# Performance work log

Hardware: AMD Instinct MI355X
Metric: run time of the kernel (lower is better)

Reference implementation:

```python
import jax, jax.numpy as jnp
import numpy as np

B = 32          # decode batch (one new token each)
KV = 4096       # kv-cache length per sequence
H = 4096        # hidden_size
NH = 32         # num query heads
NKV = 8         # num kv heads
D = 128         # head_dim
G = NH // NKV   # GQA group size
EPS = 1e-6
THETA = 1000000.0
SCALE = D ** -0.5


def _rmsnorm(x, w):
    var = jnp.mean(x * x, axis=-1, keepdims=True)
    return x * jax.lax.rsqrt(var + EPS) * w


def setup_inputs() -> dict:
    key = jax.random.key(0)
    ks = jax.random.split(key, 6)
    hidden_states = jax.random.normal(ks[0], (B, H), jnp.float32)
    k_buffer = jax.random.normal(ks[1], (B, KV, NKV, D), jnp.float32)
    v_buffer = jax.random.normal(ks[2], (B, KV, NKV, D), jnp.float32)
    wqkv = jax.random.normal(ks[3], ((NH + 2 * NKV) * D, H), jnp.float32) * 0.02
    wo = jax.random.normal(ks[4], (H, NH * D), jnp.float32) * 0.02
    q_norm_w = jnp.ones((D,), jnp.float32)
    k_norm_w = jnp.ones((D,), jnp.float32)
    # new token sits at the last cache slot; positions = kv_len-1
    position_ids = jnp.full((B,), KV - 1, jnp.int32)
    out_cache_loc = jnp.full((B,), KV - 1, jnp.int32)
    return {
        "position_ids": position_ids,
        "hidden_states": hidden_states,
        "k_buffer": k_buffer,
        "v_buffer": v_buffer,
        "out_cache_loc": out_cache_loc,
        "wqkv": wqkv,
        "wo": wo,
        "q_norm_w": q_norm_w,
        "k_norm_w": k_norm_w,
    }


def reference(position_ids, hidden_states, k_buffer, v_buffer, out_cache_loc,
              wqkv, wo, q_norm_w, k_norm_w):
    # fused QKV projection (no bias)
    qkv = hidden_states @ wqkv.T                               # [B, (NH+2NKV)*D]
    q = qkv[:, : NH * D].reshape(B, NH, D)
    k = qkv[:, NH * D : (NH + NKV) * D].reshape(B, NKV, D)
    v = qkv[:, (NH + NKV) * D :].reshape(B, NKV, D)

    # per-head RMSNorm on q and k
    q = _rmsnorm(q, q_norm_w)
    k = _rmsnorm(k, k_norm_w)

    # NeoX-style rotary embedding
    inv_freq = 1.0 / (THETA ** (jnp.arange(0, D, 2, dtype=jnp.float32) / D))
    freqs = position_ids.astype(jnp.float32)[:, None] * inv_freq  # [B, D/2]
    cos = jnp.cos(freqs)[:, None, :]
    sin = jnp.sin(freqs)[:, None, :]

    def rot(x):
        x1, x2 = jnp.split(x, 2, axis=-1)
        return jnp.concatenate([x1 * cos - x2 * sin, x2 * cos + x1 * sin], -1)

    q = rot(q)
    k = rot(k)

    # fused_set_kv_buffer: scatter roped k and pre-rope v into the cache
    b = jnp.arange(B)
    k_buffer = k_buffer.at[b, out_cache_loc].set(k)            # [B, KV, NKV, D]
    v_buffer = v_buffer.at[b, out_cache_loc].set(v)

    # GQA attention over the full cache (decode: all slots valid)
    qg = q.reshape(B, NKV, G, D)
    scores = jnp.einsum('bkgd,bskd->bkgs', qg, k_buffer) * SCALE  # [B,NKV,G,KV]
    p = jax.nn.softmax(scores, axis=-1)
    o = jnp.einsum('bkgs,bskd->bkgd', p, v_buffer).reshape(B, NH * D)

    return o @ wo.T                                            # [B, H]
```

## Files before the change

kernel.cpp:

```cpp
#include <hip/hip_runtime.h>
#include <math.h>
#include <stdint.h>

#define B_ 32
#define KV_LEN 4096
#define HID 4096
#define NH 32
#define NKV 8
#define HD 128
#define GQ 4
#define EPS 1e-6f
#define THETA 1000000.0f
#define SCALE 0.08838834764831845f
#define QKV_ROWS ((NH + 2 * NKV) * HD)
#define SPLITS 8
#define SCHUNK (KV_LEN / SPLITS)

__global__ __launch_bounds__(256, 2)
void gemm_bt(const float* __restrict__ A, const float* __restrict__ Wt,
             float* __restrict__ out, int K, int ld_out) {
    __shared__ float sh[32][256];
    const int tid  = threadIdx.x;
    const int wave = tid >> 6;
    const int lane = tid & 63;
    const int jg   = (wave & 1) * 4;
    const int bg   = (wave >> 1) * 16;
    const int j0   = blockIdx.x * 8;

    float acc[4][16];
#pragma unroll
    for (int j = 0; j < 4; ++j)
#pragma unroll
        for (int b = 0; b < 16; ++b) acc[j][b] = 0.0f;

    for (int kc = 0; kc < K; kc += 256) {
#pragma unroll
        for (int i = 0; i < 8; ++i) {
            int f   = tid + i * 256;
            int row = f >> 6;
            int c4  = f & 63;
            *reinterpret_cast<float4*>(&sh[row][c4 * 4]) =
                *reinterpret_cast<const float4*>(&A[(size_t)row * K + kc + c4 * 4]);
        }
        __syncthreads();

        float4 w4[4];
#pragma unroll
        for (int j = 0; j < 4; ++j)
            w4[j] = *reinterpret_cast<const float4*>(
                &Wt[(size_t)(j0 + jg + j) * K + kc + lane * 4]);

#pragma unroll
        for (int b = 0; b < 16; ++b) {
            float4 h4 = *reinterpret_cast<const float4*>(&sh[bg + b][lane * 4]);
#pragma unroll
            for (int j = 0; j < 4; ++j)
                acc[j][b] += w4[j].x * h4.x + w4[j].y * h4.y +
                             w4[j].z * h4.z + w4[j].w * h4.w;
        }
        __syncthreads();
    }

#pragma unroll
    for (int j = 0; j < 4; ++j) {
#pragma unroll
        for (int b = 0; b < 16; ++b) {
            float v = acc[j][b];
#pragma unroll
            for (int m = 1; m < 64; m <<= 1) v += __shfl_xor(v, m);
            if (lane == j * 16 + b)
                out[(size_t)(bg + b) * ld_out + j0 + jg + j] = v;
        }
    }
}

__global__ __launch_bounds__(64)
void qkv_post(const float* __restrict__ qkv, const int* __restrict__ pos_ids,
              const int* __restrict__ out_loc, const float* __restrict__ qw,
              const float* __restrict__ kw, float* __restrict__ qbuf,
              float* __restrict__ kbuf, float* __restrict__ vbuf) {
    const int head = blockIdx.x;
    const int b    = blockIdx.y;
    const int i    = threadIdx.x;
    const float* row = qkv + (size_t)b * QKV_ROWS + head * HD;
    float x1 = row[i], x2 = row[i + 64];

    if (head >= NH + NKV) {
        int kh  = head - NH - NKV;
        int loc = out_loc[b];
        float* dst = vbuf + (((size_t)b * KV_LEN + loc) * NKV + kh) * HD;
        dst[i] = x1;
        dst[i + 64] = x2;
        return;
    }

    float ss = x1 * x1 + x2 * x2;
#pragma unroll
    for (int m = 1; m < 64; m <<= 1) ss += __shfl_xor(ss, m);
    float r = rsqrtf(ss * (1.0f / 128.0f) + EPS);
    const float* w = (head < NH) ? qw : kw;
    float y1 = x1 * r * w[i];
    float y2 = x2 * r * w[i + 64];

    float pos = (float)pos_ids[b];
    float inv_freq = expf(-(logf(THETA) / 64.0f) * (float)i);
    float ang = pos * inv_freq;
    float c = cosf(ang), s = sinf(ang);
    float o1 = y1 * c - y2 * s;
    float o2 = y2 * c + y1 * s;

    if (head < NH) {
        float* dst = qbuf + ((size_t)b * NH + head) * HD;
        dst[i] = o1;
        dst[i + 64] = o2;
    } else {
        int kh  = head - NH;
        int loc = out_loc[b];
        float* dst = kbuf + (((size_t)b * KV_LEN + loc) * NKV + kh) * HD;
        dst[i] = o1;
        dst[i + 64] = o2;
    }
}

__global__ __launch_bounds__(256, 4)
void attn_decode(const float* __restrict__ qbuf, const float* __restrict__ kbuf,
                 const float* __restrict__ vbuf, float* __restrict__ part_o,
                 float* __restrict__ part_m, float* __restrict__ part_l) {
    const int split = blockIdx.x, h = blockIdx.y, b = blockIdx.z;
    const int tid = threadIdx.x;
    const int grp = tid >> 4;
    const int i   = tid & 15;

    float4 qa[GQ], qb[GQ];
#pragma unroll
    for (int g = 0; g < GQ; ++g) {
        const float* qp = qbuf + ((size_t)b * NH + h * GQ + g) * HD;
        qa[g] = *reinterpret_cast<const float4*>(qp + 4 * i);
        qb[g] = *reinterpret_cast<const float4*>(qp + 64 + 4 * i);
    }

    float m[GQ], l[GQ];
    float4 oa[GQ], ob[GQ];
#pragma unroll
    for (int g = 0; g < GQ; ++g) {
        m[g] = -1e30f;
        l[g] = 0.0f;
        oa[g] = make_float4(0.f, 0.f, 0.f, 0.f);
        ob[g] = make_float4(0.f, 0.f, 0.f, 0.f);
    }

    const int s0 = split * SCHUNK;
    for (int t = 0; t < SCHUNK / 16; ++t) {
        const int s = s0 + t * 16 + grp;
        const float* krow = kbuf + (((size_t)b * KV_LEN + s) * NKV + h) * HD;
        const float* vrow = vbuf + (((size_t)b * KV_LEN + s) * NKV + h) * HD;
        float4 ka = *reinterpret_cast<const float4*>(krow + 4 * i);
        float4 kb = *reinterpret_cast<const float4*>(krow + 64 + 4 * i);
        float4 va = *reinterpret_cast<const float4*>(vrow + 4 * i);
        float4 vb = *reinterpret_cast<const float4*>(vrow + 64 + 4 * i);

#pragma unroll
        for (int g = 0; g < GQ; ++g) {
            float d = ka.x * qa[g].x + ka.y * qa[g].y + ka.z * qa[g].z + ka.w * qa[g].w +
                      kb.x * qb[g].x + kb.y * qb[g].y + kb.z * qb[g].z + kb.w * qb[g].w;
            d += __shfl_xor(d, 1);
            d += __shfl_xor(d, 2);
            d += __shfl_xor(d, 4);
            d += __shfl_xor(d, 8);
            float sc = d * SCALE;
            float mn = fmaxf(m[g], sc);
            float p    = __expf(sc - mn);
            float corr = __expf(m[g] - mn);
            l[g] = l[g] * corr + p;
            oa[g].x = oa[g].x * corr + p * va.x;
            oa[g].y = oa[g].y * corr + p * va.y;
            oa[g].z = oa[g].z * corr + p * va.z;
            oa[g].w = oa[g].w * corr + p * va.w;
            ob[g].x = ob[g].x * corr + p * vb.x;
            ob[g].y = ob[g].y * corr + p * vb.y;
            ob[g].z = ob[g].z * corr + p * vb.z;
            ob[g].w = ob[g].w * corr + p * vb.w;
            m[g] = mn;
        }
    }

    __shared__ float smo[16][GQ][HD];
    __shared__ float smm[16][GQ];
    __shared__ float sml[16][GQ];
#pragma unroll
    for (int g = 0; g < GQ; ++g) {
        if (i == 0) { smm[grp][g] = m[g]; sml[grp][g] = l[g]; }
        smo[grp][g][4 * i + 0] = oa[g].x;
        smo[grp][g][4 * i + 1] = oa[g].y;
        smo[grp][g][4 * i + 2] = oa[g].z;
        smo[grp][g][4 * i + 3] = oa[g].w;
        smo[grp][g][64 + 4 * i + 0] = ob[g].x;
        smo[grp][g][64 + 4 * i + 1] = ob[g].y;
        smo[grp][g][64 + 4 * i + 2] = ob[g].z;
        smo[grp][g][64 + 4 * i + 3] = ob[g].w;
    }
    __syncthreads();

    for (int idx = tid; idx < GQ * HD; idx += 256) {
        int g = idx >> 7, d = idx & 127;
        float mstar = -1e30f;
#pragma unroll
        for (int r = 0; r < 16; ++r) mstar = fmaxf(mstar, smm[r][g]);
        float L = 0.0f, o = 0.0f;
#pragma unroll
        for (int r = 0; r < 16; ++r) {
            float w = __expf(smm[r][g] - mstar);
            L += w * sml[r][g];
            o += w * smo[r][g][d];
        }
        size_t pbase = (((size_t)b * NKV + h) * SPLITS + split) * GQ + g;
        part_o[pbase * HD + d] = o;
        if (d == 0) { part_m[pbase] = mstar; part_l[pbase] = L; }
    }
}

__global__ __launch_bounds__(128)
void attn_combine(const float* __restrict__ part_o, const float* __restrict__ part_m,
                  const float* __restrict__ part_l, float* __restrict__ attn_out) {
    const int h = blockIdx.x, b = blockIdx.y;
    const int d = threadIdx.x;
#pragma unroll
    for (int g = 0; g < GQ; ++g) {
        float mstar = -1e30f;
#pragma unroll
        for (int s = 0; s < SPLITS; ++s) {
            size_t p = (((size_t)b * NKV + h) * SPLITS + s) * GQ + g;
            mstar = fmaxf(mstar, part_m[p]);
        }
        float L = 0.0f, o = 0.0f;
#pragma unroll
        for (int s = 0; s < SPLITS; ++s) {
            size_t p = (((size_t)b * NKV + h) * SPLITS + s) * GQ + g;
            float w = __expf(part_m[p] - mstar);
            L += w * part_l[p];
            o += w * part_o[p * HD + d];
        }
        attn_out[(size_t)b * (NH * HD) + (h * GQ + g) * HD + d] = o / L;
    }
}

extern "C" void kernel_launch(void* const* d_in, const int* in_sizes, int n_in,
                              void* d_out, int out_size, void* d_ws, size_t ws_size,
                              hipStream_t stream) {
    const int*   pos    = (const int*)d_in[0];
    const float* hidden = (const float*)d_in[1];
    float*       kbuf   = (float*)d_in[2];
    float*       vbuf   = (float*)d_in[3];
    const int*   loc    = (const int*)d_in[4];
    const float* wqkv   = (const float*)d_in[5];
    const float* wo     = (const float*)d_in[6];
    const float* qnw    = (const float*)d_in[7];
    const float* knw    = (const float*)d_in[8];
    float*       out    = (float*)d_out;

    float* ws     = (float*)d_ws;
    float* qkv    = ws;
    float* qbuf   = qkv + (size_t)B_ * QKV_ROWS;
    float* part_o = qbuf + (size_t)B_ * NH * HD;
    float* part_m = part_o + (size_t)B_ * NKV * SPLITS * GQ * HD;
    float* part_l = part_m + (size_t)B_ * NKV * SPLITS * GQ;
    float* attn   = part_l + (size_t)B_ * NKV * SPLITS * GQ;

    gemm_bt<<<QKV_ROWS / 8, 256, 0, stream>>>(hidden, wqkv, qkv, HID, QKV_ROWS);
    qkv_post<<<dim3(NH + 2 * NKV, B_), 64, 0, stream>>>(qkv, pos, loc, qnw, knw,
                                                        qbuf, kbuf, vbuf);
    attn_decode<<<dim3(SPLITS, NKV, B_), 256, 0, stream>>>(qbuf, kbuf, vbuf,
                                                           part_o, part_m, part_l);
    attn_combine<<<dim3(NKV, B_), 128, 0, stream>>>(part_o, part_m, part_l, attn);
    gemm_bt<<<HID / 8, 256, 0, stream>>>(attn, wo, out, HID, HID);
}
```

Baseline: 1.166 ms.

## Double-buffer GEMM activations, prefetch KV rows, avoid cache writes, shuffle-reduce attention

The GEMM now stages activation tiles through a double-buffered LDS using global_load_lds and writes its output with one coalesced store per lane. Attention no longer scatters the new k/v into the input cache. It reads them from small side buffers when the slot matches out_cache_loc, prefetches the next K/V rows in registers, and folds SCALE into q. The per-block softmax merge uses wave shuffles before a smaller shared-memory merge. Occupancy is lowered to 3 blocks to make room for the extra prefetch registers. The cost is more register pressure, and the caller's KV cache buffers are no longer updated.

```diff
diff --git a/kernel.cpp b/kernel.cpp
--- a/kernel.cpp
+++ b/kernel.cpp
@@ -15,11 +15,12 @@
 #define QKV_ROWS ((NH + 2 * NKV) * HD)
 #define SPLITS 8
 #define SCHUNK (KV_LEN / SPLITS)
+#define NT (SCHUNK / 16)
 
 __global__ __launch_bounds__(256, 2)
 void gemm_bt(const float* __restrict__ A, const float* __restrict__ Wt,
              float* __restrict__ out, int K, int ld_out) {
-    __shared__ float sh[32][256];
+    __shared__ __align__(16) float sh[2][32][256];
     const int tid  = threadIdx.x;
     const int wave = tid >> 6;
     const int lane = tid & 63;
@@ -33,17 +34,30 @@
 #pragma unroll
         for (int b = 0; b < 16; ++b) acc[j][b] = 0.0f;
 
-    for (int kc = 0; kc < K; kc += 256) {
-#pragma unroll
-        for (int i = 0; i < 8; ++i) {
-            int f   = tid + i * 256;
-            int row = f >> 6;
-            int c4  = f & 63;
-            *reinterpret_cast<float4*>(&sh[row][c4 * 4]) =
-                *reinterpret_cast<const float4*>(&A[(size_t)row * K + kc + c4 * 4]);
-        }
-        __syncthreads();
-
+    const int nk = K >> 8;
+
+#pragma unroll
+    for (int i = 0; i < 8; ++i) {
+        const int row = 4 * i + wave;
+        __builtin_amdgcn_global_load_lds(
+            (const __attribute__((address_space(1))) void*)(A + (size_t)row * K + lane * 4),
+            (__attribute__((address_space(3))) void*)&sh[0][row][0], 16, 0, 0);
+    }
+    __syncthreads();
+
+    for (int c = 0; c < nk; ++c) {
+        const int cur = c & 1;
+        if (c + 1 < nk) {
+            const int kcn = (c + 1) << 8;
+#pragma unroll
+            for (int i = 0; i < 8; ++i) {
+                const int row = 4 * i + wave;
+                __builtin_amdgcn_global_load_lds(
+                    (const __attribute__((address_space(1))) void*)(A + (size_t)row * K + kcn + lane * 4),
+                    (__attribute__((address_space(3))) void*)&sh[cur ^ 1][row][0], 16, 0, 0);
+            }
+        }
+        const int kc = c << 8;
         float4 w4[4];
 #pragma unroll
         for (int j = 0; j < 4; ++j)
@@ -52,7 +66,7 @@
 
 #pragma unroll
         for (int b = 0; b < 16; ++b) {
-            float4 h4 = *reinterpret_cast<const float4*>(&sh[bg + b][lane * 4]);
+            float4 h4 = *reinterpret_cast<const float4*>(&sh[cur][bg + b][lane * 4]);
 #pragma unroll
             for (int j = 0; j < 4; ++j)
                 acc[j][b] += w4[j].x * h4.x + w4[j].y * h4.y +
@@ -61,6 +75,7 @@
         __syncthreads();
     }
 
+    float myv = 0.0f;
 #pragma unroll
     for (int j = 0; j < 4; ++j) {
 #pragma unroll
@@ -68,17 +83,17 @@
             float v = acc[j][b];
 #pragma unroll
             for (int m = 1; m < 64; m <<= 1) v += __shfl_xor(v, m);
-            if (lane == j * 16 + b)
-                out[(size_t)(bg + b) * ld_out + j0 + jg + j] = v;
-        }
-    }
+            if (lane == j * 16 + b) myv = v;
+        }
+    }
+    out[(size_t)(bg + (lane & 15)) * ld_out + j0 + jg + (lane >> 4)] = myv;
 }
 
 __global__ __launch_bounds__(64)
 void qkv_post(const float* __restrict__ qkv, const int* __restrict__ pos_ids,
-              const int* __restrict__ out_loc, const float* __restrict__ qw,
-              const float* __restrict__ kw, float* __restrict__ qbuf,
-              float* __restrict__ kbuf, float* __restrict__ vbuf) {
+              const float* __restrict__ qw, const float* __restrict__ kw,
+              float* __restrict__ qbuf, float* __restrict__ knew,
+              float* __restrict__ vnew) {
     const int head = blockIdx.x;
     const int b    = blockIdx.y;
     const int i    = threadIdx.x;
@@ -86,9 +101,7 @@
     float x1 = row[i], x2 = row[i + 64];
 
     if (head >= NH + NKV) {
-        int kh  = head - NH - NKV;
-        int loc = out_loc[b];
-        float* dst = vbuf + (((size_t)b * KV_LEN + loc) * NKV + kh) * HD;
+        float* dst = vnew + ((size_t)b * NKV + (head - NH - NKV)) * HD;
         dst[i] = x1;
         dst[i + 64] = x2;
         return;
@@ -111,25 +124,27 @@
 
     if (head < NH) {
         float* dst = qbuf + ((size_t)b * NH + head) * HD;
+        dst[i] = o1 * SCALE;
+        dst[i + 64] = o2 * SCALE;
+    } else {
+        float* dst = knew + ((size_t)b * NKV + (head - NH)) * HD;
         dst[i] = o1;
         dst[i + 64] = o2;
-    } else {
-        int kh  = head - NH;
-        int loc = out_loc[b];
-        float* dst = kbuf + (((size_t)b * KV_LEN + loc) * NKV + kh) * HD;
-        dst[i] = o1;
-        dst[i + 64] = o2;
-    }
-}
-
-__global__ __launch_bounds__(256, 4)
+    }
+}
+
+__global__ __launch_bounds__(256, 3)
 void attn_decode(const float* __restrict__ qbuf, const float* __restrict__ kbuf,
-                 const float* __restrict__ vbuf, float* __restrict__ part_o,
-                 float* __restrict__ part_m, float* __restrict__ part_l) {
+                 const float* __restrict__ vbuf, const float* __restrict__ knew,
+                 const float* __restrict__ vnew, const int* __restrict__ out_loc,
+                 float* __restrict__ part_o, float* __restrict__ part_m,
+                 float* __restrict__ part_l) {
     const int split = blockIdx.x, h = blockIdx.y, b = blockIdx.z;
-    const int tid = threadIdx.x;
-    const int grp = tid >> 4;
-    const int i   = tid & 15;
+    const int tid  = threadIdx.x;
+    const int wave = tid >> 6;
+    const int grp  = tid >> 4;
+    const int i    = tid & 15;
+    const int loc  = out_loc[b];
 
     float4 qa[GQ], qb[GQ];
 #pragma unroll
@@ -143,21 +158,32 @@
     float4 oa[GQ], ob[GQ];
 #pragma unroll
     for (int g = 0; g < GQ; ++g) {
-        m[g] = -1e30f;
-        l[g] = 0.0f;
+        m[g] = -1e30f; l[g] = 0.0f;
         oa[g] = make_float4(0.f, 0.f, 0.f, 0.f);
         ob[g] = make_float4(0.f, 0.f, 0.f, 0.f);
     }
 
+    const float* kn = knew + ((size_t)b * NKV + h) * HD;
+    const float* vn = vnew + ((size_t)b * NKV + h) * HD;
     const int s0 = split * SCHUNK;
-    for (int t = 0; t < SCHUNK / 16; ++t) {
-        const int s = s0 + t * 16 + grp;
-        const float* krow = kbuf + (((size_t)b * KV_LEN + s) * NKV + h) * HD;
-        const float* vrow = vbuf + (((size_t)b * KV_LEN + s) * NKV + h) * HD;
-        float4 ka = *reinterpret_cast<const float4*>(krow + 4 * i);
-        float4 kb = *reinterpret_cast<const float4*>(krow + 64 + 4 * i);
-        float4 va = *reinterpret_cast<const float4*>(vrow + 4 * i);
-        float4 vb = *reinterpret_cast<const float4*>(vrow + 64 + 4 * i);
+
+    int s = s0 + grp;
+    const float* kr = (s == loc) ? kn : kbuf + (((size_t)b * KV_LEN + s) * NKV + h) * HD;
+    const float* vr = (s == loc) ? vn : vbuf + (((size_t)b * KV_LEN + s) * NKV + h) * HD;
+    float4 ka = *reinterpret_cast<const float4*>(kr + 4 * i);
+    float4 kb = *reinterpret_cast<const float4*>(kr + 64 + 4 * i);
+    float4 va = *reinterpret_cast<const float4*>(vr + 4 * i);
+    float4 vb = *reinterpret_cast<const float4*>(vr + 64 + 4 * i);
+
+    for (int t = 0; t < NT; ++t) {
+        const int tn = (t + 1 < NT) ? t + 1 : t;
+        const int sn = s0 + tn * 16 + grp;
+        const float* krn = (sn == loc) ? kn : kbuf + (((size_t)b * KV_LEN + sn) * NKV + h) * HD;
+        const float* vrn = (sn == loc) ? vn : vbuf + (((size_t)b * KV_LEN + sn) * NKV + h) * HD;
+        float4 ka_n = *reinterpret_cast<const float4*>(krn + 4 * i);
+        float4 kb_n = *reinterpret_cast<const float4*>(krn + 64 + 4 * i);
+        float4 va_n = *reinterpret_cast<const float4*>(vrn + 4 * i);
+        float4 vb_n = *reinterpret_cast<const float4*>(vrn + 64 + 4 * i);
 
 #pragma unroll
         for (int g = 0; g < GQ; ++g) {
@@ -167,55 +193,78 @@
             d += __shfl_xor(d, 2);
             d += __shfl_xor(d, 4);
             d += __shfl_xor(d, 8);
-            float sc = d * SCALE;
-            float mn = fmaxf(m[g], sc);
-            float p    = __expf(sc - mn);
+            float mn   = fmaxf(m[g], d);
+            float p    = __expf(d - mn);
             float corr = __expf(m[g] - mn);
             l[g] = l[g] * corr + p;
-            oa[g].x = oa[g].x * corr + p * va.x;
-            oa[g].y = oa[g].y * corr + p * va.y;
-            oa[g].z = oa[g].z * corr + p * va.z;
-            oa[g].w = oa[g].w * corr + p * va.w;
-            ob[g].x = ob[g].x * corr + p * vb.x;
-            ob[g].y = ob[g].y * corr + p * vb.y;
-            ob[g].z = ob[g].z * corr + p * vb.z;
-            ob[g].w = ob[g].w * corr + p * vb.w;
+            oa[g].x = fmaf(oa[g].x, corr, p * va.x);
+            oa[g].y = fmaf(oa[g].y, corr, p * va.y);
+            oa[g].z = fmaf(oa[g].z, corr, p * va.z);
+            oa[g].w = fmaf(oa[g].w, corr, p * va.w);
+            ob[g].x = fmaf(ob[g].x, corr, p * vb.x);
+            ob[g].y = fmaf(ob[g].y, corr, p * vb.y);
+            ob[g].z = fmaf(ob[g].z, corr, p * vb.z);
+            ob[g].w = fmaf(ob[g].w, corr, p * vb.w);
             m[g] = mn;
         }
-    }
-
-    __shared__ float smo[16][GQ][HD];
-    __shared__ float smm[16][GQ];
-    __shared__ float sml[16][GQ];
-#pragma unroll
-    for (int g = 0; g < GQ; ++g) {
-        if (i == 0) { smm[grp][g] = m[g]; sml[grp][g] = l[g]; }
-        smo[grp][g][4 * i + 0] = oa[g].x;
-        smo[grp][g][4 * i + 1] = oa[g].y;
-        smo[grp][g][4 * i + 2] = oa[g].z;
-        smo[grp][g][4 * i + 3] = oa[g].w;
-        smo[grp][g][64 + 4 * i + 0] = ob[g].x;
-        smo[grp][g][64 + 4 * i + 1] = ob[g].y;
-        smo[grp][g][64 + 4 * i + 2] = ob[g].z;
-        smo[grp][g][64 + 4 * i + 3] = ob[g].w;
+        ka = ka_n; kb = kb_n; va = va_n; vb = vb_n;
+    }
+
+#pragma unroll
+    for (int off = 16; off <= 32; off <<= 1) {
+#pragma unroll
+        for (int g = 0; g < GQ; ++g) {
+            float mo = __shfl_xor(m[g], off);
+            float lo = __shfl_xor(l[g], off);
+            float M  = fmaxf(m[g], mo);
+            float cs = __expf(m[g] - M);
+            float co = __expf(mo - M);
+            l[g] = l[g] * cs + lo * co;
+            float4 t;
+            t.x = __shfl_xor(oa[g].x, off); t.y = __shfl_xor(oa[g].y, off);
+            t.z = __shfl_xor(oa[g].z, off); t.w = __shfl_xor(oa[g].w, off);
+            oa[g].x = oa[g].x * cs + t.x * co; oa[g].y = oa[g].y * cs + t.y * co;
+            oa[g].z = oa[g].z * cs + t.z * co; oa[g].w = oa[g].w * cs + t.w * co;
+            t.x = __shfl_xor(ob[g].x, off); t.y = __shfl_xor(ob[g].y, off);
+            t.z = __shfl_xor(ob[g].z, off); t.w = __shfl_xor(ob[g].w, off);
+            ob[g].x = ob[g].x * cs + t.x * co; ob[g].y = ob[g].y * cs + t.y * co;
+            ob[g].z = ob[g].z * cs + t.z * co; ob[g].w = ob[g].w * cs + t.w * co;
+            m[g] = M;
+        }
+    }
+
+    __shared__ float smo[4][GQ][HD];
+    __shared__ float smm[4][GQ];
+    __shared__ float sml[4][GQ];
+    if ((tid & 63) < 16) {
+#pragma unroll
+        for (int g = 0; g < GQ; ++g) {
+            if (i == 0) { smm[wave][g] = m[g]; sml[wave][g] = l[g]; }
+            smo[wave][g][4 * i + 0] = oa[g].x;
+            smo[wave][g][4 * i + 1] = oa[g].y;
+            smo[wave][g][4 * i + 2] = oa[g].z;
+            smo[wave][g][4 * i + 3] = oa[g].w;
+            smo[wave][g][64 + 4 * i + 0] = ob[g].x;
+            smo[wave][g][64 + 4 * i + 1] = ob[g].y;
+            smo[wave][g][64 + 4 * i + 2] = ob[g].z;
+            smo[wave][g][64 + 4 * i + 3] = ob[g].w;
+        }
     }
     __syncthreads();
 
     for (int idx = tid; idx < GQ * HD; idx += 256) {
         int g = idx >> 7, d = idx & 127;
-        float mstar = -1e30f;
-#pragma unroll
-        for (int r = 0; r < 16; ++r) mstar = fmaxf(mstar, smm[r][g]);
+        float M = fmaxf(fmaxf(smm[0][g], smm[1][g]), fmaxf(smm[2][g], smm[3][g]));
         float L = 0.0f, o = 0.0f;
 #pragma unroll
-        for (int r = 0; r < 16; ++r) {
-            float w = __expf(smm[r][g] - mstar);
-            L += w * sml[r][g];
-            o += w * smo[r][g][d];
+        for (int w = 0; w < 4; ++w) {
+            float wt = __expf(smm[w][g] - M);
+            L += wt * sml[w][g];
+            o += wt * smo[w][g][d];
         }
         size_t pbase = (((size_t)b * NKV + h) * SPLITS + split) * GQ + g;
         part_o[pbase * HD + d] = o;
-        if (d == 0) { part_m[pbase] = mstar; part_l[pbase] = L; }
+        if (d == 0) { part_m[pbase] = M; part_l[pbase] = L; }
     }
 }
 
@@ -249,8 +298,8 @@
                               hipStream_t stream) {
     const int*   pos    = (const int*)d_in[0];
     const float* hidden = (const float*)d_in[1];
-    float*       kbuf   = (float*)d_in[2];
-    float*       vbuf   = (float*)d_in[3];
+    const float* kbuf   = (const float*)d_in[2];
+    const float* vbuf   = (const float*)d_in[3];
     const int*   loc    = (const int*)d_in[4];
     const float* wqkv   = (const float*)d_in[5];
     const float* wo     = (const float*)d_in[6];
@@ -261,16 +310,19 @@
     float* ws     = (float*)d_ws;
     float* qkv    = ws;
     float* qbuf   = qkv + (size_t)B_ * QKV_ROWS;
-    float* part_o = qbuf + (size_t)B_ * NH * HD;
+    float* knew   = qbuf + (size_t)B_ * NH * HD;
+    float* vnew   = knew + (size_t)B_ * NKV * HD;
+    float* part_o = vnew + (size_t)B_ * NKV * HD;
     float* part_m = part_o + (size_t)B_ * NKV * SPLITS * GQ * HD;
     float* part_l = part_m + (size_t)B_ * NKV * SPLITS * GQ;
-    float* attn   = part_l + (size_t)B_ * NKV * SPLITS * GQ;
+    float* attnb  = part_l + (size_t)B_ * NKV * SPLITS * GQ;
 
     gemm_bt<<<QKV_ROWS / 8, 256, 0, stream>>>(hidden, wqkv, qkv, HID, QKV_ROWS);
-    qkv_post<<<dim3(NH + 2 * NKV, B_), 64, 0, stream>>>(qkv, pos, loc, qnw, knw,
-                                                        qbuf, kbuf, vbuf);
+    qkv_post<<<dim3(NH + 2 * NKV, B_), 64, 0, stream>>>(qkv, pos, qnw, knw,
+                                                        qbuf, knew, vnew);
     attn_decode<<<dim3(SPLITS, NKV, B_), 256, 0, stream>>>(qbuf, kbuf, vbuf,
+                                                           knew, vnew, loc,
                                                            part_o, part_m, part_l);
-    attn_combine<<<dim3(NKV, B_), 128, 0, stream>>>(part_o, part_m, part_l, attn);
-    gemm_bt<<<HID / 8, 256, 0, stream>>>(attn, wo, out, HID, HID);
-}
+    attn_combine<<<dim3(NKV, B_), 128, 0, stream>>>(part_o, part_m, part_l, attnb);
+    gemm_bt<<<HID / 8, 256, 0, stream>>>(attnb, wo, out, HID, HID);
+}
```

Result: no change. 1.150 ms (-1.4%).
